# Kernel tuning notes

Measured on AMD Instinct MI355X. Metric: run time of the kernel, lower is better.

## Reference

```python
import jax, jax.numpy as jnp
import numpy as np

EMBED = 1024
HEADS = 16
HEAD_DIM = EMBED // HEADS
B, L = 4, 2048


def setup_inputs() -> dict:
    key = jax.random.key(0)
    ks = jax.random.split(key, 10)
    s = 1.0 / np.sqrt(EMBED)
    x = jax.random.normal(ks[0], (B, L, EMBED), dtype=jnp.float32)
    mask = jax.random.randint(ks[1], (B, 1, L, L), 0, 2, dtype=jnp.int32)
    Wq = jax.random.normal(ks[2], (EMBED, EMBED), dtype=jnp.float32) * s
    Wk = jax.random.normal(ks[3], (EMBED, EMBED), dtype=jnp.float32) * s
    Wv = jax.random.normal(ks[4], (EMBED, EMBED), dtype=jnp.float32) * s
    Wo = jax.random.normal(ks[5], (EMBED, EMBED), dtype=jnp.float32) * s
    bq = jnp.zeros((EMBED,), jnp.float32)
    bk = jnp.zeros((EMBED,), jnp.float32)
    bv = jnp.zeros((EMBED,), jnp.float32)
    bo = jnp.zeros((EMBED,), jnp.float32)
    return {"x": x, "mask": mask, "Wq": Wq, "bq": bq, "Wk": Wk, "bk": bk,
            "Wv": Wv, "bv": bv, "Wo": Wo, "bo": bo}


def reference(x, mask, Wq, bq, Wk, bk, Wv, bv, Wo, bo):
    n, l, _ = x.shape
    q = (x @ Wq + bq).reshape(n, l, HEADS, HEAD_DIM)
    k = (x @ Wk + bk).reshape(n, l, HEADS, HEAD_DIM)
    v = (x @ Wv + bv).reshape(n, l, HEADS, HEAD_DIM)
    # [n, h, q, k] scores
    energy = jnp.einsum('nqhd,nkhd->nhqk', q, k)
    energy = jnp.where(mask == 0, jnp.float32(-1e20), energy)
    attn = jax.nn.softmax(energy / jnp.sqrt(jnp.float32(HEAD_DIM)), axis=-1)
    out = jnp.einsum('nhqk,nkhd->nqhd', attn, v).reshape(n, l, EMBED)
    return out @ Wo + bo
```

## Files before the change

### kernel.cpp

```cpp
#include <hip/hip_runtime.h>
#include <hip/hip_bf16.h>

#define EMBED 1024
#define HEADS 16
#define HDIM 64
#define BATCH 4
#define SEQ 2048
#define ROWS (BATCH * SEQ)
#define LOG2E 1.4426950408889634f

typedef __attribute__((ext_vector_type(8))) short bf16x8;
typedef __attribute__((ext_vector_type(4))) float f32x4;

#define MFMA16(a, b, c) __builtin_amdgcn_mfma_f32_16x16x32_bf16(a, b, c, 0, 0, 0)

__device__ __forceinline__ unsigned short f2bf(float f) {
    union { float f; unsigned int u; } x; x.f = f;
    unsigned int r = x.u + 0x7fffu + ((x.u >> 16) & 1u);
    return (unsigned short)(r >> 16);
}

__device__ __forceinline__ unsigned int pkbf(float a, float b) {
#if __has_builtin(__builtin_amdgcn_cvt_pk_bf16_f32)
    auto v = __builtin_amdgcn_cvt_pk_bf16_f32(a, b);
    unsigned int u; __builtin_memcpy(&u, &v, 4); return u;
#else
    union { __hip_bfloat162 h; unsigned int u; } c;
    c.h = __float22bfloat162_rn(make_float2(a, b)); return c.u;
#endif
}

__device__ __forceinline__ void gl2lds(const unsigned short* g, unsigned short* l) {
    __builtin_amdgcn_global_load_lds(
        (const __attribute__((address_space(1))) unsigned int*)g,
        (__attribute__((address_space(3))) unsigned int*)l, 16, 0, 0);
}

#define XBLK 8192
#define MBLK 16384
#define WBLK 4096

__global__ __launch_bounds__(256) void prep_kernel(
    const float* __restrict__ x, const int* __restrict__ mask,
    const float* __restrict__ W0, const float* __restrict__ W1,
    const float* __restrict__ W2, const float* __restrict__ W3,
    unsigned short* __restrict__ Xb, unsigned char* __restrict__ m8,
    unsigned short* __restrict__ Wt)
{
    __shared__ float t[32][33];
    const int bid = blockIdx.x;
    if (bid < XBLK) {
        int i = (bid * 256 + threadIdx.x) * 4;
        float4 v = *(const float4*)(x + i);
        uint2 o; o.x = pkbf(v.x, v.y); o.y = pkbf(v.z, v.w);
        *(uint2*)(Xb + i) = o;
    } else if (bid < XBLK + MBLK) {
        int i = ((bid - XBLK) * 256 + threadIdx.x) * 4;
        int4 v = *(const int4*)(mask + i);
        uchar4 o;
        o.x = v.x ? 0xFF : 0; o.y = v.y ? 0xFF : 0;
        o.z = v.z ? 0xFF : 0; o.w = v.w ? 0xFF : 0;
        *(uchar4*)(m8 + i) = o;
    } else {
        int f = bid - XBLK - MBLK;
        int z = f >> 10, rem = f & 1023;
        const float* W = (z == 0) ? W0 : (z == 1) ? W1 : (z == 2) ? W2 : W3;
        unsigned short* o = Wt + (size_t)z * EMBED * EMBED;
        int tx = threadIdx.x & 31, ty = threadIdx.x >> 5;
        int bx = (rem & 31) * 32, by = (rem >> 5) * 32;
#pragma unroll
        for (int r = 0; r < 32; r += 8)
            t[ty + r][tx] = W[(size_t)(by + ty + r) * EMBED + bx + tx];
        __syncthreads();
#pragma unroll
        for (int r = 0; r < 32; r += 8)
            o[(size_t)(bx + ty + r) * EMBED + by + tx] = f2bf(t[tx][ty + r]);
    }
}

__device__ __forceinline__ void gemm_bf16_body(
    const unsigned short* __restrict__ A, const unsigned short* __restrict__ Bt,
    const float* __restrict__ bias,
    float* __restrict__ outF, unsigned short* __restrict__ outB, float scale,
    int vmode, int m0, int n0)
{
    __shared__ unsigned short As[128][64];
    __shared__ unsigned short Bs[128][64];
    const int tid = threadIdx.x;
    const int lane = tid & 63, wid = tid >> 6;
    const int ln = lane & 15, lg = lane >> 4;
    const int wy = wid >> 1, wx = wid & 1;
    const int r0 = wid * 32 + (lane >> 3);
    const int scol = (((lane & 7) ^ ((lane >> 3) & 7)) << 3);
    const unsigned short* Ap = A + (size_t)(m0 + r0) * EMBED + scol;
    const unsigned short* Bp = Bt + (size_t)(n0 + r0) * EMBED + scol;
    unsigned short* lA = &As[wid * 32][0];
    unsigned short* lB = &Bs[wid * 32][0];

    f32x4 acc[4][4];
#pragma unroll
    for (int i = 0; i < 4; i++)
#pragma unroll
        for (int j = 0; j < 4; j++) acc[i][j] = (f32x4){0.f, 0.f, 0.f, 0.f};

    for (int k0 = 0; k0 < EMBED; k0 += 64) {
        __syncthreads();
#pragma unroll
        for (int is = 0; is < 4; is++) {
            gl2lds(Ap + k0 + (size_t)(is * 8) * EMBED, lA + is * 8 * 64);
            gl2lds(Bp + k0 + (size_t)(is * 8) * EMBED, lB + is * 8 * 64);
        }
        __syncthreads();
        bf16x8 af[2][4], bfr[2][4];
#pragma unroll
        for (int s = 0; s < 2; s++) {
#pragma unroll
            for (int mi = 0; mi < 4; mi++)
                af[s][mi] = *(const bf16x8*)
                    &As[wy * 64 + mi * 16 + ln][(((lg + 4 * s) ^ (ln & 7)) << 3)];
#pragma unroll
            for (int nj = 0; nj < 4; nj++)
                bfr[s][nj] = *(const bf16x8*)
                    &Bs[wx * 64 + nj * 16 + ln][(((lg + 4 * s) ^ (ln & 7)) << 3)];
        }
#pragma unroll
        for (int s = 0; s < 2; s++)
#pragma unroll
            for (int mi = 0; mi < 4; mi++)
#pragma unroll
                for (int nj = 0; nj < 4; nj++)
                    acc[mi][nj] = MFMA16(af[s][mi], bfr[s][nj], acc[mi][nj]);
    }

#pragma unroll
    for (int mi = 0; mi < 4; mi++) {
#pragma unroll
        for (int nj = 0; nj < 4; nj++) {
            int row = m0 + wy * 64 + mi * 16 + lg * 4;
            int col = n0 + wx * 64 + nj * 16 + ln;
            float bv = bias[col];
            if (vmode) {
                int bb = row >> 11, s = row & (SEQ - 1);
                int hh = col >> 6, dd = col & 63;
                unsigned short* dst = outB +
                    ((size_t)((bb * HEADS + hh) * HDIM + dd)) * SEQ + s;
                uint2 pw;
                pw.x = pkbf(acc[mi][nj][0] + bv, acc[mi][nj][1] + bv);
                pw.y = pkbf(acc[mi][nj][2] + bv, acc[mi][nj][3] + bv);
                *(uint2*)dst = pw;
            } else {
#pragma unroll
                for (int r = 0; r < 4; r++) {
                    float v = (acc[mi][nj][r] + bv) * scale;
                    if (outF) outF[(size_t)(row + r) * EMBED + col] = v;
                    else      outB[(size_t)(row + r) * EMBED + col] = f2bf(v);
                }
            }
        }
    }
}

__global__ __launch_bounds__(256) void qkv_gemm_kernel(
    const unsigned short* __restrict__ Xb, const unsigned short* __restrict__ Wt,
    const float* __restrict__ bq, const float* __restrict__ bk,
    const float* __restrict__ bv,
    unsigned short* __restrict__ Qb, unsigned short* __restrict__ Kb,
    unsigned short* __restrict__ Vt)
{
    const int bid = blockIdx.x;
    const int xcd = bid & 7;
    const int idx = bid >> 3;
    const int bx  = idx & 7;
    const int yi  = (idx >> 3) & 7;
    const int z   = idx >> 6;
    const int by  = xcd * 8 + yi;

    const unsigned short* Bt = Wt + (size_t)z * EMBED * EMBED;
    const float* bias = (z == 0) ? bq : (z == 1) ? bk : bv;
    unsigned short* out = (z == 0) ? Qb : (z == 1) ? Kb : Vt;
    float scale = (z == 0) ? 0.125f * LOG2E : 1.0f;
    gemm_bf16_body(Xb, Bt, bias, nullptr, out, scale, z == 2,
                   by * 128, bx * 128);
}

__global__ __launch_bounds__(256) void out_gemm_kernel(
    const unsigned short* __restrict__ Ob, const unsigned short* __restrict__ Wto,
    const float* __restrict__ bo, float* __restrict__ out)
{
    const int bid = blockIdx.x;
    const int xcd = bid & 7;
    const int idx = bid >> 3;
    const int bx  = idx & 7;
    const int yi  = idx >> 3;
    const int by  = xcd * 8 + yi;
    gemm_bf16_body(Ob, Wto, bo, out, nullptr, 1.0f, 0, by * 128, bx * 128);
}

__global__ __launch_bounds__(256) void attn_mfma_kernel(
    const unsigned short* __restrict__ Qb, const unsigned short* __restrict__ Kb,
    const unsigned short* __restrict__ Vt, const unsigned char* __restrict__ mask8,
    unsigned short* __restrict__ Ob)
{
    __shared__ unsigned short Ks[64][64];
    __shared__ unsigned short Vs[64][64];
    __shared__ unsigned short Ps[4][32][64];
    const int tid = threadIdx.x;
    const int lane = tid & 63, wid = tid >> 6;
    const int ln = lane & 15, lg = lane >> 4;
    const int b = blockIdx.z, h = blockIdx.y;
    const int q0 = blockIdx.x * 128 + wid * 32;

    bf16x8 qf[2][2];
#pragma unroll
    for (int mi = 0; mi < 2; mi++)
#pragma unroll
        for (int ks = 0; ks < 2; ks++)
            qf[mi][ks] = *(const bf16x8*)(Qb +
                (size_t)(b * SEQ + q0 + mi * 16 + ln) * EMBED + h * HDIM + ks * 32 + lg * 8);

    bf16x8 ones;
#pragma unroll
    for (int i = 0; i < 8; i++) ones[i] = (short)0x3F80;

    f32x4 o[2][4];
#pragma unroll
    for (int mi = 0; mi < 2; mi++)
#pragma unroll
        for (int dj = 0; dj < 4; dj++) o[mi][dj] = (f32x4){0.f, 0.f, 0.f, 0.f};
    f32x4 lacc[2] = {(f32x4){0.f, 0.f, 0.f, 0.f}, (f32x4){0.f, 0.f, 0.f, 0.f}};

    const int srow = tid >> 3;
    const int scolKV = (((tid & 7) ^ ((tid >> 3) & 7)) << 3);
    const unsigned short* Kp = Kb + (size_t)(b * SEQ + srow) * EMBED + h * HDIM + scolKV;
    const unsigned short* Vp = Vt + (size_t)((b * HEADS + h) * HDIM + srow) * SEQ + scolKV;
    unsigned short* lK = &Ks[srow & ~7][0];
    unsigned short* lV = &Vs[srow & ~7][0];

    const unsigned char* mq0 = mask8 + (size_t)b * SEQ * SEQ + (size_t)(q0 + ln) * SEQ;
    const unsigned char* mq1 = mq0 + (size_t)16 * SEQ;

    const int swk = ((lg ^ (ln & 7)) << 3);

    int pwr[4], prd[2];
#pragma unroll
    for (int nj = 0; nj < 4; nj++)
        pwr[nj] = (((2 * nj + (lg >> 1)) ^ (ln & 7)) << 3) + ((lg & 1) << 2);
#pragma unroll
    for (int ks = 0; ks < 2; ks++)
        prd[ks] = ((4 * ks + lg) ^ (ln & 7)) << 3;
    unsigned short* ps0 = &Ps[wid][ln][0];
    unsigned short* ps1 = &Ps[wid][16 + ln][0];

    for (int kt = 0; kt < SEQ; kt += 64) {
        unsigned int mw[2][4];
#pragma unroll
        for (int mi = 0; mi < 2; mi++) {
            const unsigned char* mq = (mi ? mq1 : mq0) + kt;
#pragma unroll
            for (int nj = 0; nj < 4; nj++)
                mw[mi][nj] = *(const unsigned int*)(mq + nj * 16 + lg * 4);
        }

        __syncthreads();
        gl2lds(Kp + (size_t)kt * EMBED, lK);
        gl2lds(Kp + (size_t)(kt + 32) * EMBED, lK + 32 * 64);
        gl2lds(Vp + kt, lV);
        gl2lds(Vp + (size_t)32 * SEQ + kt, lV + 32 * 64);
        __syncthreads();

        f32x4 S[2][4];
#pragma unroll
        for (int nj = 0; nj < 4; nj++) {
            bf16x8 k0 = *(const bf16x8*)&Ks[nj * 16 + ln][swk];
            bf16x8 k1 = *(const bf16x8*)&Ks[nj * 16 + ln][swk ^ 32];
#pragma unroll
            for (int mi = 0; mi < 2; mi++) {
                f32x4 t2 = (f32x4){0.f, 0.f, 0.f, 0.f};
                t2 = MFMA16(k0, qf[mi][0], t2);
                t2 = MFMA16(k1, qf[mi][1], t2);
                S[mi][nj] = t2;
            }
        }

#pragma unroll
        for (int mi = 0; mi < 2; mi++) {
            unsigned short* psb = mi ? ps1 : ps0;
#pragma unroll
            for (int nj = 0; nj < 4; nj++) {
                float p0 = __builtin_amdgcn_exp2f(S[mi][nj][0]);
                float p1 = __builtin_amdgcn_exp2f(S[mi][nj][1]);
                float p2 = __builtin_amdgcn_exp2f(S[mi][nj][2]);
                float p3 = __builtin_amdgcn_exp2f(S[mi][nj][3]);
                unsigned int m = mw[mi][nj];
                unsigned int d0 = __builtin_amdgcn_perm(0u, m, 0x01010000u);
                unsigned int d1 = __builtin_amdgcn_perm(0u, m, 0x03030202u);
                uint2 pw;
                pw.x = pkbf(p0, p1) & d0;
                pw.y = pkbf(p2, p3) & d1;
                *(uint2*)(psb + pwr[nj]) = pw;
            }
        }

#pragma unroll
        for (int ks = 0; ks < 2; ks++) {
            bf16x8 p0 = *(const bf16x8*)(ps0 + prd[ks]);
            bf16x8 p1 = *(const bf16x8*)(ps1 + prd[ks]);
            lacc[0] = MFMA16(p0, ones, lacc[0]);
            lacc[1] = MFMA16(p1, ones, lacc[1]);
#pragma unroll
            for (int dj = 0; dj < 4; dj++) {
                bf16x8 vf = *(const bf16x8*)&Vs[dj * 16 + ln][swk ^ (ks << 5)];
                o[0][dj] = MFMA16(p0, vf, o[0][dj]);
                o[1][dj] = MFMA16(p1, vf, o[1][dj]);
            }
        }
    }

#pragma unroll
    for (int mi = 0; mi < 2; mi++) {
        float l0 = 1.0f / lacc[mi][0];
        float l1 = 1.0f / lacc[mi][1];
        float l2 = 1.0f / lacc[mi][2];
        float l3 = 1.0f / lacc[mi][3];
#pragma unroll
        for (int dj = 0; dj < 4; dj++) {
            unsigned short* op = Ob + (size_t)(b * SEQ + q0 + mi * 16 + lg * 4) * EMBED
                                    + h * HDIM + dj * 16 + ln;
            op[0]         = f2bf(o[mi][dj][0] * l0);
            op[EMBED]     = f2bf(o[mi][dj][1] * l1);
            op[2 * EMBED] = f2bf(o[mi][dj][2] * l2);
            op[3 * EMBED] = f2bf(o[mi][dj][3] * l3);
        }
    }
}

extern "C" void kernel_launch(void* const* d_in, const int* in_sizes, int n_in,
                              void* d_out, int out_size, void* d_ws, size_t ws_size,
                              hipStream_t stream)
{
    const float* x  = (const float*)d_in[0];
    const int* mask = (const int*)d_in[1];
    const float* Wq = (const float*)d_in[2];
    const float* bq = (const float*)d_in[3];
    const float* Wk = (const float*)d_in[4];
    const float* bk = (const float*)d_in[5];
    const float* Wv = (const float*)d_in[6];
    const float* bv = (const float*)d_in[7];
    const float* Wo = (const float*)d_in[8];
    const float* bo = (const float*)d_in[9];
    float* outp = (float*)d_out;

    char* ws = (char*)d_ws;
    unsigned short* Wt = (unsigned short*)(ws);
    unsigned char*  m8 = (unsigned char*)(ws + ((size_t)8 << 20));
    unsigned short* Xb = (unsigned short*)(ws + ((size_t)24 << 20));
    unsigned short* Ob = Xb;
    unsigned short* Qb = (unsigned short*)(ws + ((size_t)40 << 20));
    unsigned short* Kb = (unsigned short*)(ws + ((size_t)56 << 20));
    unsigned short* Vt = (unsigned short*)(ws + ((size_t)72 << 20));

    prep_kernel<<<XBLK + MBLK + WBLK, 256, 0, stream>>>(
        x, mask, Wq, Wk, Wv, Wo, Xb, m8, Wt);
    qkv_gemm_kernel<<<1536, 256, 0, stream>>>(
        Xb, Wt, bq, bk, bv, Qb, Kb, Vt);
    attn_mfma_kernel<<<dim3(SEQ / 128, HEADS, BATCH), 256, 0, stream>>>(
        Qb, Kb, Vt, m8, Ob);
    out_gemm_kernel<<<512, 256, 0, stream>>>(
        Ob, Wt + (size_t)3 * EMBED * EMBED, bo, outp);
}
```

Before: 387.2 us.

## Keep softmax probabilities in registers and remap attention grid across XCDs

The attention kernel no longer round-trips the probability tile through LDS. It reorders the V tile's columns when loading it through registers, so the MFMA C-layout of P can feed the PV MFMA directly as the A operand. The grid is flattened to 1D and remapped so blocks sharing a batch-head land on the same XCD, which is meant to improve L2 reuse of K and V. In exchange, V is now staged through registers with regular loads instead of direct global-to-LDS copies, which can add latency and register pressure.

After: 380.9 us, median of 2. About the same (-1.6%).

```diff
diff --git a/kernel.cpp b/kernel.cpp
--- a/kernel.cpp
+++ b/kernel.cpp
@@ -203,12 +203,17 @@
 {
     __shared__ unsigned short Ks[64][64];
     __shared__ unsigned short Vs[64][64];
-    __shared__ unsigned short Ps[4][32][64];
     const int tid = threadIdx.x;
     const int lane = tid & 63, wid = tid >> 6;
     const int ln = lane & 15, lg = lane >> 4;
-    const int b = blockIdx.z, h = blockIdx.y;
-    const int q0 = blockIdx.x * 128 + wid * 32;
+
+    const int bid = blockIdx.x;
+    const int xcd = bid & 7;
+    const int i5 = bid >> 3;
+    const int qx = i5 & 15;
+    const int bh = xcd * 8 + (i5 >> 4);
+    const int h = bh & 15, b = bh >> 4;
+    const int q0 = qx * 128 + wid * 32;
 
     bf16x8 qf[2][2];
 #pragma unroll
@@ -230,26 +235,26 @@
     f32x4 lacc[2] = {(f32x4){0.f, 0.f, 0.f, 0.f}, (f32x4){0.f, 0.f, 0.f, 0.f}};
 
     const int srow = tid >> 3;
-    const int scolKV = (((tid & 7) ^ ((tid >> 3) & 7)) << 3);
-    const unsigned short* Kp = Kb + (size_t)(b * SEQ + srow) * EMBED + h * HDIM + scolKV;
-    const unsigned short* Vp = Vt + (size_t)((b * HEADS + h) * HDIM + srow) * SEQ + scolKV;
+    const int scolK = (((tid & 7) ^ ((tid >> 3) & 7)) << 3);
+    const unsigned short* Kp = Kb + (size_t)(b * SEQ + srow) * EMBED + h * HDIM + scolK;
     unsigned short* lK = &Ks[srow & ~7][0];
-    unsigned short* lV = &Vs[srow & ~7][0];
+
+    const int vrow = tid >> 2, vu = tid & 3;
+    const unsigned short* Vp = Vt + (size_t)((b * HEADS + h) * HDIM + vrow) * SEQ + 4 * vu;
+    unsigned short* vdst = &Vs[vrow][0];
+    const int vw0 = ((vu ^ (vrow & 7)) << 3);
+    const int vw1 = (((vu + 4) ^ (vrow & 7)) << 3);
 
     const unsigned char* mq0 = mask8 + (size_t)b * SEQ * SEQ + (size_t)(q0 + ln) * SEQ;
     const unsigned char* mq1 = mq0 + (size_t)16 * SEQ;
 
     const int swk = ((lg ^ (ln & 7)) << 3);
-
-    int pwr[4], prd[2];
-#pragma unroll
-    for (int nj = 0; nj < 4; nj++)
-        pwr[nj] = (((2 * nj + (lg >> 1)) ^ (ln & 7)) << 3) + ((lg & 1) << 2);
+    int vrd[2];
 #pragma unroll
     for (int ks = 0; ks < 2; ks++)
-        prd[ks] = ((4 * ks + lg) ^ (ln & 7)) << 3;
-    unsigned short* ps0 = &Ps[wid][ln][0];
-    unsigned short* ps1 = &Ps[wid][16 + ln][0];
+        vrd[ks] = ((4 * ks + lg) ^ (ln & 7)) << 3;
+
+    union U8 { bf16x8 v; unsigned int w[4]; };
 
     for (int kt = 0; kt < SEQ; kt += 64) {
         unsigned int mw[2][4];
@@ -261,11 +266,20 @@
                 mw[mi][nj] = *(const unsigned int*)(mq + nj * 16 + lg * 4);
         }
 
+        uint2 v0 = *(const uint2*)(Vp + kt);
+        uint2 v1 = *(const uint2*)(Vp + kt + 16);
+        uint2 v2 = *(const uint2*)(Vp + kt + 32);
+        uint2 v3 = *(const uint2*)(Vp + kt + 48);
+
         __syncthreads();
         gl2lds(Kp + (size_t)kt * EMBED, lK);
         gl2lds(Kp + (size_t)(kt + 32) * EMBED, lK + 32 * 64);
-        gl2lds(Vp + kt, lV);
-        gl2lds(Vp + (size_t)32 * SEQ + kt, lV + 32 * 64);
+        {
+            uint4 w0; w0.x = v0.x; w0.y = v0.y; w0.z = v1.x; w0.w = v1.y;
+            uint4 w1; w1.x = v2.x; w1.y = v2.y; w1.z = v3.x; w1.w = v3.y;
+            *(uint4*)(vdst + vw0) = w0;
+            *(uint4*)(vdst + vw1) = w1;
+        }
         __syncthreads();
 
         f32x4 S[2][4];
@@ -282,34 +296,34 @@
             }
         }
 
-#pragma unroll
-        for (int mi = 0; mi < 2; mi++) {
-            unsigned short* psb = mi ? ps1 : ps0;
-#pragma unroll
-            for (int nj = 0; nj < 4; nj++) {
-                float p0 = __builtin_amdgcn_exp2f(S[mi][nj][0]);
-                float p1 = __builtin_amdgcn_exp2f(S[mi][nj][1]);
-                float p2 = __builtin_amdgcn_exp2f(S[mi][nj][2]);
-                float p3 = __builtin_amdgcn_exp2f(S[mi][nj][3]);
-                unsigned int m = mw[mi][nj];
-                unsigned int d0 = __builtin_amdgcn_perm(0u, m, 0x01010000u);
-                unsigned int d1 = __builtin_amdgcn_perm(0u, m, 0x03030202u);
-                uint2 pw;
-                pw.x = pkbf(p0, p1) & d0;
-                pw.y = pkbf(p2, p3) & d1;
-                *(uint2*)(psb + pwr[nj]) = pw;
-            }
-        }
+        U8 pf[2][2];
+#pragma unroll
+        for (int mi = 0; mi < 2; mi++)
+#pragma unroll
+            for (int ks = 0; ks < 2; ks++)
+#pragma unroll
+                for (int hf = 0; hf < 2; hf++) {
+                    const int nj = 2 * ks + hf;
+                    float p0 = __builtin_amdgcn_exp2f(S[mi][nj][0]);
+                    float p1 = __builtin_amdgcn_exp2f(S[mi][nj][1]);
+                    float p2 = __builtin_amdgcn_exp2f(S[mi][nj][2]);
+                    float p3 = __builtin_amdgcn_exp2f(S[mi][nj][3]);
+                    unsigned int m = mw[mi][nj];
+                    unsigned int d0 = __builtin_amdgcn_perm(0u, m, 0x01010000u);
+                    unsigned int d1 = __builtin_amdgcn_perm(0u, m, 0x03030202u);
+                    pf[mi][ks].w[2 * hf]     = pkbf(p0, p1) & d0;
+                    pf[mi][ks].w[2 * hf + 1] = pkbf(p2, p3) & d1;
+                }
 
 #pragma unroll
         for (int ks = 0; ks < 2; ks++) {
-            bf16x8 p0 = *(const bf16x8*)(ps0 + prd[ks]);
-            bf16x8 p1 = *(const bf16x8*)(ps1 + prd[ks]);
+            bf16x8 p0 = pf[0][ks].v;
+            bf16x8 p1 = pf[1][ks].v;
             lacc[0] = MFMA16(p0, ones, lacc[0]);
             lacc[1] = MFMA16(p1, ones, lacc[1]);
 #pragma unroll
             for (int dj = 0; dj < 4; dj++) {
-                bf16x8 vf = *(const bf16x8*)&Vs[dj * 16 + ln][swk ^ (ks << 5)];
+                bf16x8 vf = *(const bf16x8*)&Vs[dj * 16 + ln][vrd[ks]];
                 o[0][dj] = MFMA16(p0, vf, o[0][dj]);
                 o[1][dj] = MFMA16(p1, vf, o[1][dj]);
             }
@@ -363,7 +377,7 @@
         x, mask, Wq, Wk, Wv, Wo, Xb, m8, Wt);
     qkv_gemm_kernel<<<1536, 256, 0, stream>>>(
         Xb, Wt, bq, bk, bv, Qb, Kb, Vt);
-    attn_mfma_kernel<<<dim3(SEQ / 128, HEADS, BATCH), 256, 0, stream>>>(
+    attn_mfma_kernel<<<1024, 256, 0, stream>>>(
         Qb, Kb, Vt, m8, Ob);
     out_gemm_kernel<<<512, 256, 0, stream>>>(
         Ob, Wt + (size_t)3 * EMBED * EMBED, bo, outp);
```
